# Optimization experiments

Measured on AMD Instinct MI355X. Metric: run time of the kernel, lower is better.

The kernel has to match this reference:

```python
import jax, jax.numpy as jnp
import numpy as np

N, DIM, T, V = 32, 256, 120, 25
H, HD = 8, 32            # num_heads, head_dim
MAX_HOP = 4
SCALE = HD ** -0.5


def setup_inputs() -> dict:
    key = jax.random.key(0)
    ks = jax.random.split(key, 9)
    x = jax.random.normal(ks[0], (N, DIM, T, V), jnp.float32)
    e = jax.random.normal(ks[1], (N, DIM, T, V), jnp.float32)
    # 1x1 conv weights (trunc_normal std=0.02 in the original init)
    W_kv = jax.random.normal(ks[2], (2 * DIM, DIM), jnp.float32) * 0.02
    W_q = jax.random.normal(ks[3], (DIM, DIM), jnp.float32) * 0.02
    W_proj = jax.random.normal(ks[4], (DIM, DIM), jnp.float32) * 0.02
    b_proj = jnp.zeros((DIM,), jnp.float32)
    rpe = jax.random.normal(ks[5], (MAX_HOP + 1, DIM), jnp.float32) * 0.02
    w1 = jax.random.normal(ks[6], (H, HD), jnp.float32) * 0.02
    # outer initialized as per-head identity (plus noise so grads are interesting)
    outer = jnp.broadcast_to(jnp.eye(V, dtype=jnp.float32), (H, V, V)) \
        + 0.1 * jax.random.normal(ks[7], (H, V, V), jnp.float32)
    alpha = 0.1 * jax.random.normal(ks[8], (1,), jnp.float32)
    idx = jnp.arange(V)
    hops = jnp.minimum(jnp.abs(idx[:, None] - idx[None, :]), MAX_HOP).astype(jnp.int32)
    return dict(x=x, e=e, W_kv=W_kv, W_q=W_q, W_proj=W_proj, b_proj=b_proj,
                rpe=rpe, w1=w1, outer=outer, alpha=alpha, hops=hops)


def reference(x, e, W_kv, W_q, W_proj, b_proj, rpe, w1, outer, alpha, hops):
    n, c, t, v = x.shape
    # 1x1 convs == channel matmuls
    kv = jnp.einsum('nctv,dc->ndtv', x, W_kv)                    # [N,2*DIM,T,V]
    kv = kv.reshape(n, 2, H, HD, t, v).transpose(1, 0, 4, 2, 5, 3)  # [2,N,T,H,V,HD]
    k, vv = kv[0], kv[1]
    q = jnp.einsum('nctv,dc->ndtv', x, W_q)
    q = q.reshape(n, H, HD, t, v).transpose(0, 3, 1, 4, 2)       # [N,T,H,V,HD]
    # content score
    attn = jnp.einsum('bthnc,bthmc->bthnm', q, k)                # [N,T,H,V,V]
    # hop relative-position bias
    k_r = rpe[hops].reshape(v, v, H, HD)                         # [V,V,H,HD]
    attn = attn + jnp.einsum('bthnc,nmhc->bthnm', q, k_r)
    # group term
    e_k = e.reshape(n, H, HD, t, v).transpose(0, 3, 1, 4, 2)     # [N,T,H,V,HD]
    attn = attn + jnp.einsum('bthnc,bthmc->bthnm', q, e_k)
    # group bias (broadcast over query index)
    attn = attn + jnp.einsum('hc,bthmc->bthm', w1, e_k)[..., None, :]
    attn = jax.nn.softmax(attn * SCALE, axis=-1)
    # outer/adjacency fusion then weighted V
    out = jnp.einsum('bthnm,bthmc->bthnc', alpha[0] * attn + outer, vv)
    # [N,T,H,V,HD] -> [N,T,H,HD,V] -> [N,T,DIM,V] -> [N,DIM,T,V]
    out = out.transpose(0, 1, 2, 4, 3).reshape(n, t, H * HD, v).transpose(0, 2, 1, 3)
    out = jnp.einsum('nctv,dc->ndtv', out, W_proj) + b_proj[None, :, None, None]
    return out
```

## Files before the change

### kernel.cpp

```cpp
#include <hip/hip_runtime.h>

typedef __attribute__((ext_vector_type(8))) short bf16x8;
typedef __attribute__((ext_vector_type(4))) float f32x4;
typedef unsigned short u16;
typedef unsigned int u32;

#define SCALE_ 0.17677669529663687f
#define MFMA(a,b,c) __builtin_amdgcn_mfma_f32_16x16x32_bf16(a,b,c,0,0,0)

__device__ __forceinline__ u16 f2bf(float f){
    u32 u = __float_as_uint(f);
    u = (u + 0x7FFFu + ((u >> 16) & 1u)) >> 16;
    return (u16)u;
}
__device__ __forceinline__ float bf2f(u32 h){ return __uint_as_float(h << 16); }
__device__ __forceinline__ u32 pk2(float a, float b){ return (u32)f2bf(a) | ((u32)f2bf(b) << 16); }

__device__ __forceinline__ bf16x8 frag8(uint2 p0, uint2 p1, int kg, int l15){
    const int s0 = ((kg & 1) << 5) + l15;
    const int s1 = s0 + 16;
    u32 a0 = (u32)__shfl((int)p0.x, s0, 64);
    u32 a1 = (u32)__shfl((int)p0.y, s0, 64);
    u32 a2 = (u32)__shfl((int)p0.x, s1, 64);
    u32 a3 = (u32)__shfl((int)p0.y, s1, 64);
    u32 b0 = (u32)__shfl((int)p1.x, s0, 64);
    u32 b1 = (u32)__shfl((int)p1.y, s0, 64);
    u32 b2 = (u32)__shfl((int)p1.x, s1, 64);
    u32 b3 = (u32)__shfl((int)p1.y, s1, 64);
    const bool hi = (kg >= 2);
    union { u32 u[4]; bf16x8 v; } r;
    r.u[0] = hi ? b0 : a0; r.u[1] = hi ? b1 : a1;
    r.u[2] = hi ? b2 : a2; r.u[3] = hi ? b3 : a3;
    return r.v;
}

#define PG_OFF_ 333312
#define NPAGES_ ((size_t)3840*8*2624)
#define BIAS_U16_ (PG_OFF_ + NPAGES_)

__global__ void prep_kernel(const float* __restrict__ Wkv, const float* __restrict__ Wq,
                            const float* __restrict__ Wproj, const float* __restrict__ rpe,
                            const float* __restrict__ w1, u16* __restrict__ wpk)
{
    int i = blockIdx.x * 256 + threadIdx.x;
    if (i < 65536)        wpk[i] = f2bf(Wq[i]);
    else if (i < 196608)  wpk[i] = f2bf(Wkv[i - 65536]);
    else if (i < 262144)  wpk[i] = f2bf(Wproj[i - 196608]);
    else if (i < 263424){
        int j = i - 262144;
        int jj = j >> 8, h = (j >> 5) & 7, hd = j & 31;
        wpk[i] = f2bf(rpe[jj*256 + h*32 + hd]);
    }
    else if (i < 263680)  wpk[i] = f2bf(w1[i - 263424]);
    else if (i < 267776){
        int j = i - 263680;
        int r = j >> 8, c = j & 255;
        float v = (r < 8 && (c >> 5) == r) ? w1[r*32 + (c & 31)] : 0.f;
        wpk[i] = f2bf(v);
    }
    else if (i < 333312){
        int j = i - 267776;
        int h = j >> 13;
        int r = j & 8191;
        int coct = r >> 8, hd = (r >> 3) & 31, clo = r & 7;
        wpk[i] = f2bf(Wkv[(size_t)(256 + h*32 + hd) * 256 + coct*8 + clo]);
    }
}

__launch_bounds__(512)
__global__ void qkv_gemm(const float* __restrict__ x, const float* __restrict__ e,
                         const u16* __restrict__ wpk, u16* __restrict__ pages,
                         float* __restrict__ bias_ws)
{
    __shared__ __align__(16) u16 xt[25664];

    const int tid = threadIdx.x;
    const int w = tid >> 6, lane = tid & 63;
    const int l15 = lane & 15, kg = lane >> 4;
    const int wg = ((int)blockIdx.x & 7) * 360 + ((int)blockIdx.x >> 3);
    const int sec = wg / 960, cb = wg % 960;
    const int n = cb / 30, tg = cb % 30;
    const f32x4 zf = {0.f, 0.f, 0.f, 0.f};

    const float* xb = x + (size_t)n*768000 + tg*100;
    for (int i = tid; i < 3200; i += 512){
        int col = i % 100, coct = i / 100;
        const float* xc = xb + (size_t)(coct*8)*3000 + col;
        u32 p[4];
        #pragma unroll
        for (int r = 0; r < 4; ++r)
            p[r] = pk2(xc[(2*r)*3000], xc[(2*r+1)*3000]);
        *(uint4*)&xt[(coct*100 + col)*8] = *(const uint4*)p;
    }
    __syncthreads();

    f32x4 acc[2][8];
    #pragma unroll
    for (int m = 0; m < 2; ++m)
        #pragma unroll
        for (int f = 0; f < 8; ++f) acc[m][f] = zf;

    const u16* wrow = wpk + (size_t)(sec*256 + w*32 + l15) * 256;
    #pragma unroll
    for (int ks = 0; ks < 8; ++ks){
        bf16x8 a0 = *(const bf16x8*)(wrow + ks*32 + kg*8);
        bf16x8 a1 = *(const bf16x8*)(wrow + 4096 + ks*32 + kg*8);
        #pragma unroll
        for (int f = 0; f < 8; ++f){
            int col = (f>>1)*25 + (f&1)*16 + l15;
            bf16x8 b = *(const bf16x8*)&xt[((ks*4+kg)*100 + col)*8];
            acc[0][f] = MFMA(a0, b, acc[0][f]);
            acc[1][f] = MFMA(a1, b, acc[1][f]);
        }
    }

    if (sec == 1){
        __syncthreads();
        const float* ebp = e + (size_t)n*768000 + tg*100;
        for (int i = tid; i < 3200; i += 512){
            int col = i % 100, coct = i / 100;
            const float* ec = ebp + (size_t)(coct*8)*3000 + col;
            u32 p[4];
            #pragma unroll
            for (int r = 0; r < 4; ++r)
                p[r] = pk2(ec[(2*r)*3000], ec[(2*r+1)*3000]);
            *(uint4*)&xt[(coct*100 + col)*8] = *(const uint4*)p;
        }
        __syncthreads();
        #pragma unroll
        for (int m = 0; m < 2; ++m){
            int c0 = w*32 + m*16 + kg*4;
            #pragma unroll
            for (int f = 0; f < 8; ++f){
                int col = (f>>1)*25 + (f&1)*16 + l15;
                uint2 ev = *(const uint2*)&xt[((c0>>3)*100 + col)*8 + (c0&7)];
                acc[m][f][0] += bf2f(ev.x & 0xFFFFu);
                acc[m][f][1] += bf2f(ev.x >> 16);
                acc[m][f][2] += bf2f(ev.y & 0xFFFFu);
                acc[m][f][3] += bf2f(ev.y >> 16);
            }
        }
    }

    const int secoff = (sec == 0) ? 0 : (sec == 1 ? 800 : 1600);
    #pragma unroll
    for (int m = 0; m < 2; ++m){
        #pragma unroll
        for (int f = 0; f < 8; ++f){
            int tt = f >> 1, a = (f&1)*16 + l15;
            if (a < 25){
                size_t nt = (size_t)(n*120 + tg*4 + tt);
                u16* pg = pages + (nt*8 + w)*2624 + secoff;
                int hd0 = m*16 + kg*4;
                if (sec < 2){
                    uint2 val; val.x = pk2(acc[m][f][0], acc[m][f][1]);
                    val.y = pk2(acc[m][f][2], acc[m][f][3]);
                    *(uint2*)&pg[((hd0>>3)*25 + a)*8 + (hd0&7)] = val;
                } else {
                    #pragma unroll
                    for (int r = 0; r < 4; ++r)
                        pg[((a>>3)*32 + hd0 + r)*8 + (a&7)] = f2bf(acc[m][f][r]);
                }
            }
        }
    }

    if (sec == 1 && w == 0){
        f32x4 bacc[8];
        #pragma unroll
        for (int f = 0; f < 8; ++f) bacc[f] = zf;
        const u16* w1f = wpk + 263680 + l15*256;
        #pragma unroll
        for (int ks = 0; ks < 8; ++ks){
            bf16x8 a = *(const bf16x8*)(w1f + ks*32 + kg*8);
            #pragma unroll
            for (int f = 0; f < 8; ++f){
                int col = (f>>1)*25 + (f&1)*16 + l15;
                bf16x8 b = *(const bf16x8*)&xt[((ks*4+kg)*100 + col)*8];
                bacc[f] = MFMA(a, b, bacc[f]);
            }
        }
        if (kg < 2){
            #pragma unroll
            for (int f = 0; f < 8; ++f){
                int tt = f >> 1, a = (f&1)*16 + l15;
                if (a < 25){
                    int nt = n*120 + tg*4 + tt;
                    #pragma unroll
                    for (int r = 0; r < 4; ++r)
                        bias_ws[(size_t)nt*256 + (kg*4+r)*32 + a] = bacc[f][r];
                }
            }
        }
    }
}

__launch_bounds__(512)
__global__ void attn_proj(const float* __restrict__ outer, const float* __restrict__ alpha,
                          const float* __restrict__ bproj, const u16* __restrict__ wpk,
                          const u16* __restrict__ pages, const float* __restrict__ bias_ws,
                          float* __restrict__ out)
{
    __shared__ __align__(16) u16 opk[6656 + 64];

    const int tid = threadIdx.x;
    const int w = tid >> 6, lane = tid & 63;
    const int l15 = lane & 15, kg = lane >> 4;
    const int wg = ((int)blockIdx.x & 7) * 480 + ((int)blockIdx.x >> 3);
    const int n = wg / 120, t = wg % 120;
    const float alpha0 = alpha[0];
    const f32x4 zf = {0.f, 0.f, 0.f, 0.f};
    const int h = w;
    const u16* pg = pages + ((size_t)wg*8 + h)*2624;

    bf16x8 fq0  = *(const bf16x8*)&pg[(kg*25 + l15)*8];
    bf16x8 fq1  = *(const bf16x8*)&pg[(kg*25 + 16 + l15)*8];
    bf16x8 fke0 = *(const bf16x8*)&pg[800 + (kg*25 + l15)*8];
    bf16x8 fke1;
    if (l15 < 9)       fke1 = *(const bf16x8*)&pg[800 + (kg*25 + 16 + l15)*8];
    else if (l15 <= 13) fke1 = *(const bf16x8*)(wpk + 262144 + ((l15-9)*8 + h)*32 + kg*8);
    else { union { u32 u[4]; bf16x8 v; } z; z.u[0]=z.u[1]=z.u[2]=z.u[3]=0; fke1 = z.v; }

    f32x4 sc[2][2];
    sc[0][0] = MFMA(fke0, fq0, zf);
    sc[0][1] = MFMA(fke0, fq1, zf);
    sc[1][0] = MFMA(fke1, fq0, zf);
    sc[1][1] = MFMA(fke1, fq1, zf);

    float bias01[2];
    bias01[0] = bias_ws[(size_t)wg*256 + h*32 + l15];
    bias01[1] = bias_ws[(size_t)wg*256 + h*32 + 16 + l15];

    uint2 P_G[2][2];
    #pragma unroll
    for (int nt = 0; nt < 2; ++nt){
        const int a = nt*16 + l15;
        f32x4 s0 = sc[0][nt], s1 = sc[1][nt];
        float rr0 = __shfl(s1[1], 32 + l15, 64);
        float rr1 = __shfl(s1[2], 32 + l15, 64);
        float rr2 = __shfl(s1[3], 32 + l15, 64);
        float rr3 = __shfl(s1[0], 48 + l15, 64);
        float rr4 = __shfl(s1[1], 48 + l15, 64);
        float tv[8];
        #pragma unroll
        for (int mt = 0; mt < 2; ++mt)
            #pragma unroll
            for (int r = 0; r < 4; ++r){
                int b = mt*16 + kg*4 + r;
                float sval = mt ? s1[r] : s0[r];
                float bb = __shfl(bias01[mt], (lane & 48) + (b & 15), 64);
                int d = a - b; d = d < 0 ? -d : d; if (d > 4) d = 4;
                float rj = d==0?rr0 : d==1?rr1 : d==2?rr2 : d==3?rr3 : rr4;
                float tt = (sval + rj + bb) * SCALE_;
                tv[mt*4+r] = (b < 25) ? tt : -1e30f;
            }
        float m = tv[0];
        #pragma unroll
        for (int i = 1; i < 8; ++i) m = fmaxf(m, tv[i]);
        m = fmaxf(m, __shfl_xor(m, 16, 64));
        m = fmaxf(m, __shfl_xor(m, 32, 64));
        float ex[8], sm = 0.f;
        #pragma unroll
        for (int i = 0; i < 8; ++i){ ex[i] = __expf(tv[i] - m); sm += ex[i]; }
        sm += __shfl_xor(sm, 16, 64);
        sm += __shfl_xor(sm, 32, 64);
        const float inv = alpha0 / sm;
        float g[8];
        #pragma unroll
        for (int mt = 0; mt < 2; ++mt)
            #pragma unroll
            for (int r = 0; r < 4; ++r){
                int b = mt*16 + kg*4 + r;
                float ov = (a < 25 && b < 25) ? outer[((size_t)h*25 + a)*25 + b] : 0.f;
                g[mt*4+r] = (b < 25) ? ex[mt*4+r]*inv + ov : 0.f;
            }
        uint2 pg0; pg0.x = pk2(g[0], g[1]); pg0.y = pk2(g[2], g[3]);
        uint2 pg1; pg1.x = pk2(g[4], g[5]); pg1.y = pk2(g[6], g[7]);
        P_G[nt][0] = pg0; P_G[nt][1] = pg1;
    }

    {
        bf16x8 fv0 = *(const bf16x8*)&pg[1600 + (kg*32 + l15)*8];
        bf16x8 fv1 = *(const bf16x8*)&pg[1600 + (kg*32 + 16 + l15)*8];
        bf16x8 fg0 = frag8(P_G[0][0], P_G[0][1], kg, l15);
        bf16x8 fg1 = frag8(P_G[1][0], P_G[1][1], kg, l15);
        f32x4 o[2][2];
        o[0][0] = MFMA(fv0, fg0, zf); o[0][1] = MFMA(fv0, fg1, zf);
        o[1][0] = MFMA(fv1, fg0, zf); o[1][1] = MFMA(fv1, fg1, zf);
        #pragma unroll
        for (int mt = 0; mt < 2; ++mt)
            #pragma unroll
            for (int nt = 0; nt < 2; ++nt){
                int a = nt*16 + l15;
                if (a < 25){
                    int coct = h*4 + mt*2 + (kg>>1);
                    u32* dst = (u32*)&opk[(coct*26 + a)*8 + (kg&1)*4];
                    dst[0] = pk2(o[mt][nt][0], o[mt][nt][1]);
                    dst[1] = pk2(o[mt][nt][2], o[mt][nt][3]);
                }
            }
    }
    __syncthreads();

    {
        f32x4 pc[2][2];
        #pragma unroll
        for (int i = 0; i < 2; ++i){ pc[i][0] = zf; pc[i][1] = zf; }
        #pragma unroll
        for (int ks = 0; ks < 8; ++ks){
            bf16x8 pb0 = *(const bf16x8*)&opk[((ks*4+kg)*26 + l15)*8];
            bf16x8 pb1 = *(const bf16x8*)&opk[((ks*4+kg)*26 + 16 + l15)*8];
            #pragma unroll
            for (int i = 0; i < 2; ++i){
                bf16x8 aw = *(const bf16x8*)(wpk + 196608 +
                                (size_t)(w*32 + i*16 + l15)*256 + ks*32 + kg*8);
                pc[i][0] = MFMA(aw, pb0, pc[i][0]);
                pc[i][1] = MFMA(aw, pb1, pc[i][1]);
            }
        }
        #pragma unroll
        for (int i = 0; i < 2; ++i){
            const int d = w*32 + i*16 + kg*4;
            float b0 = bproj[d], b1 = bproj[d+1], b2 = bproj[d+2], b3 = bproj[d+3];
            #pragma unroll
            for (int nt = 0; nt < 2; ++nt){
                int v = nt*16 + l15;
                if (v < 25){
                    float* op = out + (size_t)n*768000 + (size_t)d*3000 + t*25 + v;
                    op[0]    = pc[i][nt][0] + b0;
                    op[3000] = pc[i][nt][1] + b1;
                    op[6000] = pc[i][nt][2] + b2;
                    op[9000] = pc[i][nt][3] + b3;
                }
            }
        }
    }
}

__launch_bounds__(512, 4)
__global__ void mhsa_main(const float* __restrict__ x, const float* __restrict__ e,
                          const float* __restrict__ outer, const float* __restrict__ alpha,
                          const float* __restrict__ bproj, const u16* __restrict__ wpk,
                          float* __restrict__ out)
{
    __shared__ __align__(16) u16 smem[6656*3 + 64];
    u16* xs  = smem;
    u16* es  = smem + 6656;
    u16* opk = smem + 13312;

    const int tid = threadIdx.x;
    const int w = tid >> 6, lane = tid & 63;
    const int l15 = lane & 15, kg = lane >> 4;
    const int wg = (blockIdx.x & 7) * 480 + (blockIdx.x >> 3);
    const int n = wg / 120, t = wg % 120;
    const float alpha0 = alpha[0];
    const f32x4 zf = {0.f, 0.f, 0.f, 0.f};

    const float* xb = x + (size_t)n*768000 + t*25;
    const float* eb = e + (size_t)n*768000 + t*25;
    for (int i = tid; i < 6400; i += 512){
        int c = i / 25, v = i - c*25;
        int a16 = ((c>>3)*26 + v)*8 + (c&7);
        xs[a16] = f2bf(xb[c*3000 + v]);
        es[a16] = f2bf(eb[c*3000 + v]);
    }
    __syncthreads();

    {
        const int h = w;
        f32x4 cq[2][2], ck[2][2];
        #pragma unroll
        for (int i = 0; i < 2; ++i)
            #pragma unroll
            for (int j = 0; j < 2; ++j){ cq[i][j] = zf; ck[i][j] = zf; }
        {
            const u16* wq0 = wpk + (size_t)(h*32 + l15)*256;
            const u16* wk0 = wpk + 65536 + (size_t)(h*32 + l15)*256;
            #pragma unroll
            for (int ks = 0; ks < 8; ++ks){
                bf16x8 b0 = *(const bf16x8*)&xs[((ks*4+kg)*26 + l15)*8];
                bf16x8 b1 = *(const bf16x8*)&xs[((ks*4+kg)*26 + 16 + l15)*8];
                bf16x8 aq0 = *(const bf16x8*)(wq0 + ks*32 + kg*8);
                bf16x8 aq1 = *(const bf16x8*)(wq0 + 4096 + ks*32 + kg*8);
                bf16x8 ak0 = *(const bf16x8*)(wk0 + ks*32 + kg*8);
                bf16x8 ak1 = *(const bf16x8*)(wk0 + 4096 + ks*32 + kg*8);
                cq[0][0]=MFMA(aq0,b0,cq[0][0]); cq[0][1]=MFMA(aq0,b1,cq[0][1]);
                cq[1][0]=MFMA(aq1,b0,cq[1][0]); cq[1][1]=MFMA(aq1,b1,cq[1][1]);
                ck[0][0]=MFMA(ak0,b0,ck[0][0]); ck[0][1]=MFMA(ak0,b1,ck[0][1]);
                ck[1][0]=MFMA(ak1,b0,ck[1][0]); ck[1][1]=MFMA(ak1,b1,ck[1][1]);
            }
        }
        uint2 P_q[2][2], P_k[2][2];
        #pragma unroll
        for (int mt = 0; mt < 2; ++mt)
            #pragma unroll
            for (int nt = 0; nt < 2; ++nt){
                int coct = h*4 + mt*2 + (kg>>1);
                uint2 ev = *(const uint2*)&es[(coct*26 + nt*16 + l15)*8 + (kg&1)*4];
                ck[mt][nt][0] += bf2f(ev.x & 0xFFFFu);
                ck[mt][nt][1] += bf2f(ev.x >> 16);
                ck[mt][nt][2] += bf2f(ev.y & 0xFFFFu);
                ck[mt][nt][3] += bf2f(ev.y >> 16);
                uint2 pq; pq.x = pk2(cq[mt][nt][0], cq[mt][nt][1]);
                pq.y = pk2(cq[mt][nt][2], cq[mt][nt][3]);
                P_q[nt][mt] = pq;
                uint2 pk; pk.x = pk2(ck[mt][nt][0], ck[mt][nt][1]);
                pk.y = pk2(ck[mt][nt][2], ck[mt][nt][3]);
                P_k[nt][mt] = pk;
            }
        float bias01[2];
        {
            bf16x8 aw1 = *(const bf16x8*)(wpk + 263424 + h*32 + kg*8);
            bf16x8 be0 = *(const bf16x8*)&es[((h*4+kg)*26 + l15)*8];
            bf16x8 be1 = *(const bf16x8*)&es[((h*4+kg)*26 + 16 + l15)*8];
            f32x4 cb0 = MFMA(aw1, be0, zf);
            f32x4 cb1 = MFMA(aw1, be1, zf);
            bias01[0] = cb0[0]; bias01[1] = cb1[0];
        }
        f32x4 cv[2][2];
        #pragma unroll
        for (int i = 0; i < 2; ++i)
            #pragma unroll
            for (int j = 0; j < 2; ++j) cv[i][j] = zf;
        {
            const u16* wvt = wpk + 267776 + h*8192;
            #pragma unroll
            for (int ks = 0; ks < 8; ++ks){
                bf16x8 a0 = *(const bf16x8*)&xs[((ks*4+kg)*26 + l15)*8];
                bf16x8 a1 = *(const bf16x8*)&xs[((ks*4+kg)*26 + 16 + l15)*8];
                bf16x8 bv0 = *(const bf16x8*)&wvt[((ks*4+kg)*32 + l15)*8];
                bf16x8 bv1 = *(const bf16x8*)&wvt[((ks*4+kg)*32 + 16 + l15)*8];
                cv[0][0]=MFMA(a0,bv0,cv[0][0]); cv[0][1]=MFMA(a0,bv1,cv[0][1]);
                cv[1][0]=MFMA(a1,bv0,cv[1][0]); cv[1][1]=MFMA(a1,bv1,cv[1][1]);
            }
        }
        #pragma unroll
        for (int nt = 0; nt < 2; ++nt)
            #pragma unroll
            for (int r = 0; r < 4; ++r)
                cv[1][nt][r] = (kg*4 + r < 9) ? cv[1][nt][r] : 0.f;
        uint2 P_v[2][2];
        #pragma unroll
        for (int mt = 0; mt < 2; ++mt)
            #pragma unroll
            for (int nt = 0; nt < 2; ++nt){
                uint2 pv; pv.x = pk2(cv[mt][nt][0], cv[mt][nt][1]);
                pv.y = pk2(cv[mt][nt][2], cv[mt][nt][3]);
                P_v[nt][mt] = pv;
            }
        bf16x8 fq0  = frag8(P_q[0][0], P_q[0][1], kg, l15);
        bf16x8 fq1  = frag8(P_q[1][0], P_q[1][1], kg, l15);
        bf16x8 fke0 = frag8(P_k[0][0], P_k[0][1], kg, l15);
        bf16x8 fke1 = frag8(P_k[1][0], P_k[1][1], kg, l15);
        if (l15 >= 9){
            if (l15 <= 13)
                fke1 = *(const bf16x8*)(wpk + 262144 + ((l15-9)*8 + h)*32 + kg*8);
            else {
                union { u32 u[4]; bf16x8 v; } z; z.u[0]=z.u[1]=z.u[2]=z.u[3]=0;
                fke1 = z.v;
            }
        }
        f32x4 sc[2][2];
        sc[0][0] = MFMA(fke0, fq0, zf);
        sc[0][1] = MFMA(fke0, fq1, zf);
        sc[1][0] = MFMA(fke1, fq0, zf);
        sc[1][1] = MFMA(fke1, fq1, zf);
        uint2 P_G[2][2];
        #pragma unroll
        for (int nt = 0; nt < 2; ++nt){
            const int a = nt*16 + l15;
            f32x4 s0 = sc[0][nt], s1 = sc[1][nt];
            float rr0 = __shfl(s1[1], 32 + l15, 64);
            float rr1 = __shfl(s1[2], 32 + l15, 64);
            float rr2 = __shfl(s1[3], 32 + l15, 64);
            float rr3 = __shfl(s1[0], 48 + l15, 64);
            float rr4 = __shfl(s1[1], 48 + l15, 64);
            float tv[8];
            #pragma unroll
            for (int mt = 0; mt < 2; ++mt)
                #pragma unroll
                for (int r = 0; r < 4; ++r){
                    int b = mt*16 + kg*4 + r;
                    float sval = mt ? s1[r] : s0[r];
                    float bb = __shfl(bias01[mt], (lane & 48) + (b & 15), 64);
                    int d = a - b; d = d < 0 ? -d : d; if (d > 4) d = 4;
                    float rj = d==0?rr0 : d==1?rr1 : d==2?rr2 : d==3?rr3 : rr4;
                    float tt = (sval + rj + bb) * SCALE_;
                    tv[mt*4+r] = (b < 25) ? tt : -1e30f;
                }
            float m = tv[0];
            #pragma unroll
            for (int i = 1; i < 8; ++i) m = fmaxf(m, tv[i]);
            m = fmaxf(m, __shfl_xor(m, 16, 64));
            m = fmaxf(m, __shfl_xor(m, 32, 64));
            float ex[8], sm = 0.f;
            #pragma unroll
            for (int i = 0; i < 8; ++i){ ex[i] = __expf(tv[i] - m); sm += ex[i]; }
            sm += __shfl_xor(sm, 16, 64);
            sm += __shfl_xor(sm, 32, 64);
            const float inv = alpha0 / sm;
            float g[8];
            #pragma unroll
            for (int mt = 0; mt < 2; ++mt)
                #pragma unroll
                for (int r = 0; r < 4; ++r){
                    int b = mt*16 + kg*4 + r;
                    float ov = (a < 25 && b < 25) ? outer[((size_t)h*25 + a)*25 + b] : 0.f;
                    g[mt*4+r] = (b < 25) ? ex[mt*4+r]*inv + ov : 0.f;
                }
            uint2 pg0; pg0.x = pk2(g[0], g[1]); pg0.y = pk2(g[2], g[3]);
            uint2 pg1; pg1.x = pk2(g[4], g[5]); pg1.y = pk2(g[6], g[7]);
            P_G[nt][0] = pg0; P_G[nt][1] = pg1;
        }
        {
            bf16x8 fv0 = frag8(P_v[0][0], P_v[0][1], kg, l15);
            bf16x8 fv1 = frag8(P_v[1][0], P_v[1][1], kg, l15);
            bf16x8 fg0 = frag8(P_G[0][0], P_G[0][1], kg, l15);
            bf16x8 fg1 = frag8(P_G[1][0], P_G[1][1], kg, l15);
            f32x4 o[2][2];
            o[0][0] = MFMA(fv0, fg0, zf); o[0][1] = MFMA(fv0, fg1, zf);
            o[1][0] = MFMA(fv1, fg0, zf); o[1][1] = MFMA(fv1, fg1, zf);
            #pragma unroll
            for (int mt = 0; mt < 2; ++mt)
                #pragma unroll
                for (int nt = 0; nt < 2; ++nt){
                    int a = nt*16 + l15;
                    if (a < 25){
                        int coct = h*4 + mt*2 + (kg>>1);
                        u32* dst = (u32*)&opk[(coct*26 + a)*8 + (kg&1)*4];
                        dst[0] = pk2(o[mt][nt][0], o[mt][nt][1]);
                        dst[1] = pk2(o[mt][nt][2], o[mt][nt][3]);
                    }
                }
        }
    }
    __syncthreads();

    {
        f32x4 pc[2][2];
        #pragma unroll
        for (int i = 0; i < 2; ++i){ pc[i][0] = zf; pc[i][1] = zf; }
        #pragma unroll
        for (int ks = 0; ks < 8; ++ks){
            bf16x8 pb0 = *(const bf16x8*)&opk[((ks*4+kg)*26 + l15)*8];
            bf16x8 pb1 = *(const bf16x8*)&opk[((ks*4+kg)*26 + 16 + l15)*8];
            #pragma unroll
            for (int i = 0; i < 2; ++i){
                bf16x8 aw = *(const bf16x8*)(wpk + 196608 +
                                (size_t)(w*32 + i*16 + l15)*256 + ks*32 + kg*8);
                pc[i][0] = MFMA(aw, pb0, pc[i][0]);
                pc[i][1] = MFMA(aw, pb1, pc[i][1]);
            }
        }
        #pragma unroll
        for (int i = 0; i < 2; ++i){
            const int d = w*32 + i*16 + kg*4;
            float b0 = bproj[d], b1 = bproj[d+1], b2 = bproj[d+2], b3 = bproj[d+3];
            #pragma unroll
            for (int nt = 0; nt < 2; ++nt){
                int v = nt*16 + l15;
                if (v < 25){
                    float* op = out + (size_t)n*768000 + (size_t)d*3000 + t*25 + v;
                    op[0]    = pc[i][nt][0] + b0;
                    op[3000] = pc[i][nt][1] + b1;
                    op[6000] = pc[i][nt][2] + b2;
                    op[9000] = pc[i][nt][3] + b3;
                }
            }
        }
    }
}

extern "C" void kernel_launch(void* const* d_in, const int* in_sizes, int n_in,
                              void* d_out, int out_size, void* d_ws, size_t ws_size,
                              hipStream_t stream) {
    (void)in_sizes; (void)n_in; (void)out_size;
    const float* x     = (const float*)d_in[0];
    const float* e     = (const float*)d_in[1];
    const float* Wkv   = (const float*)d_in[2];
    const float* Wq    = (const float*)d_in[3];
    const float* Wproj = (const float*)d_in[4];
    const float* bproj = (const float*)d_in[5];
    const float* rpe   = (const float*)d_in[6];
    const float* w1    = (const float*)d_in[7];
    const float* outer = (const float*)d_in[8];
    const float* alpha = (const float*)d_in[9];
    float* out = (float*)d_out;
    u16* wpk = (u16*)d_ws;

    prep_kernel<<<1302, 256, 0, stream>>>(Wkv, Wq, Wproj, rpe, w1, wpk);

    const size_t need = (size_t)BIAS_U16_ * 2 + (size_t)3840*256*4 + 4096;
    if (ws_size >= need){
        u16* pages = wpk + PG_OFF_;
        float* bias_ws = (float*)(wpk + BIAS_U16_);
        qkv_gemm<<<2880, 512, 0, stream>>>(x, e, wpk, pages, bias_ws);
        attn_proj<<<3840, 512, 0, stream>>>(outer, alpha, bproj, wpk, pages, bias_ws, out);
    } else {
        mhsa_main<<<3840, 512, 0, stream>>>(x, e, outer, alpha, bproj, wpk, out);
    }
}
```

Baseline: 278.8 us.

## Split qkv_gemm into smaller 30-column, half-head-range blocks for more parallelism

Restructures the QKV projection kernel so each 256-thread block handles 30 flattened (t,v) columns and half of the output channels of one section, instead of 100 columns and all channels with 512 threads. The grid grows from 2880 to 19200 blocks and LDS per block shrinks, aiming for higher occupancy and better load balance. It also adds occupancy hints to launch_bounds on both kernels. In exchange, each x/e tile is now loaded and converted six times across sections and halves, raising global read traffic, and MFMA work per block is much smaller.

```diff
diff --git a/kernel.cpp b/kernel.cpp
--- a/kernel.cpp
+++ b/kernel.cpp
@@ -67,48 +67,48 @@
     }
 }
 
-__launch_bounds__(512)
+__launch_bounds__(256, 8)
 __global__ void qkv_gemm(const float* __restrict__ x, const float* __restrict__ e,
                          const u16* __restrict__ wpk, u16* __restrict__ pages,
                          float* __restrict__ bias_ws)
 {
-    __shared__ __align__(16) u16 xt[25664];
+    __shared__ __align__(16) u16 xt[7696];
 
     const int tid = threadIdx.x;
     const int w = tid >> 6, lane = tid & 63;
     const int l15 = lane & 15, kg = lane >> 4;
-    const int wg = ((int)blockIdx.x & 7) * 360 + ((int)blockIdx.x >> 3);
-    const int sec = wg / 960, cb = wg % 960;
-    const int n = cb / 30, tg = cb % 30;
+    const int wg = ((int)blockIdx.x & 7) * 2400 + ((int)blockIdx.x >> 3);
+    const int n = wg / 600, rr = wg % 600;
+    const int tg = rr / 6, sr = rr % 6;
+    const int sec = sr >> 1, h2 = sr & 1;
     const f32x4 zf = {0.f, 0.f, 0.f, 0.f};
 
-    const float* xb = x + (size_t)n*768000 + tg*100;
-    for (int i = tid; i < 3200; i += 512){
-        int col = i % 100, coct = i / 100;
+    const float* xb = x + (size_t)n*768000 + tg*30;
+    for (int i = tid; i < 960; i += 256){
+        int col = i % 30, coct = i / 30;
         const float* xc = xb + (size_t)(coct*8)*3000 + col;
         u32 p[4];
         #pragma unroll
-        for (int r = 0; r < 4; ++r)
-            p[r] = pk2(xc[(2*r)*3000], xc[(2*r+1)*3000]);
-        *(uint4*)&xt[(coct*100 + col)*8] = *(const uint4*)p;
+        for (int r2 = 0; r2 < 4; ++r2)
+            p[r2] = pk2(xc[(2*r2)*3000], xc[(2*r2+1)*3000]);
+        *(uint4*)&xt[(coct*30 + col)*8] = *(const uint4*)p;
     }
     __syncthreads();
 
-    f32x4 acc[2][8];
+    f32x4 acc[2][2];
     #pragma unroll
     for (int m = 0; m < 2; ++m)
         #pragma unroll
-        for (int f = 0; f < 8; ++f) acc[m][f] = zf;
-
-    const u16* wrow = wpk + (size_t)(sec*256 + w*32 + l15) * 256;
+        for (int f = 0; f < 2; ++f) acc[m][f] = zf;
+
+    const u16* wrow = wpk + (size_t)(sec*256 + h2*128 + w*32 + l15) * 256;
     #pragma unroll
     for (int ks = 0; ks < 8; ++ks){
         bf16x8 a0 = *(const bf16x8*)(wrow + ks*32 + kg*8);
         bf16x8 a1 = *(const bf16x8*)(wrow + 4096 + ks*32 + kg*8);
         #pragma unroll
-        for (int f = 0; f < 8; ++f){
-            int col = (f>>1)*25 + (f&1)*16 + l15;
-            bf16x8 b = *(const bf16x8*)&xt[((ks*4+kg)*100 + col)*8];
+        for (int f = 0; f < 2; ++f){
+            bf16x8 b = *(const bf16x8*)&xt[((ks*4+kg)*30 + f*16 + l15)*8];
             acc[0][f] = MFMA(a0, b, acc[0][f]);
             acc[1][f] = MFMA(a1, b, acc[1][f]);
         }
@@ -116,24 +116,23 @@
 
     if (sec == 1){
         __syncthreads();
-        const float* ebp = e + (size_t)n*768000 + tg*100;
-        for (int i = tid; i < 3200; i += 512){
-            int col = i % 100, coct = i / 100;
+        const float* ebp = e + (size_t)n*768000 + tg*30;
+        for (int i = tid; i < 960; i += 256){
+            int col = i % 30, coct = i / 30;
             const float* ec = ebp + (size_t)(coct*8)*3000 + col;
             u32 p[4];
             #pragma unroll
-            for (int r = 0; r < 4; ++r)
-                p[r] = pk2(ec[(2*r)*3000], ec[(2*r+1)*3000]);
-            *(uint4*)&xt[(coct*100 + col)*8] = *(const uint4*)p;
+            for (int r2 = 0; r2 < 4; ++r2)
+                p[r2] = pk2(ec[(2*r2)*3000], ec[(2*r2+1)*3000]);
+            *(uint4*)&xt[(coct*30 + col)*8] = *(const uint4*)p;
         }
         __syncthreads();
         #pragma unroll
         for (int m = 0; m < 2; ++m){
-            int c0 = w*32 + m*16 + kg*4;
-            #pragma unroll
-            for (int f = 0; f < 8; ++f){
-                int col = (f>>1)*25 + (f&1)*16 + l15;
-                uint2 ev = *(const uint2*)&xt[((c0>>3)*100 + col)*8 + (c0&7)];
+            int c0 = h2*128 + w*32 + m*16 + kg*4;
+            #pragma unroll
+            for (int f = 0; f < 2; ++f){
+                uint2 ev = *(const uint2*)&xt[((c0>>3)*30 + f*16 + l15)*8 + (c0&7)];
                 acc[m][f][0] += bf2f(ev.x & 0xFFFFu);
                 acc[m][f][1] += bf2f(ev.x >> 16);
                 acc[m][f][2] += bf2f(ev.y & 0xFFFFu);
@@ -143,14 +142,17 @@
     }
 
     const int secoff = (sec == 0) ? 0 : (sec == 1 ? 800 : 1600);
+    const int h = h2*4 + w;
     #pragma unroll
     for (int m = 0; m < 2; ++m){
         #pragma unroll
-        for (int f = 0; f < 8; ++f){
-            int tt = f >> 1, a = (f&1)*16 + l15;
-            if (a < 25){
-                size_t nt = (size_t)(n*120 + tg*4 + tt);
-                u16* pg = pages + (nt*8 + w)*2624 + secoff;
+        for (int f = 0; f < 2; ++f){
+            int sl = f*16 + l15;
+            if (sl < 30){
+                int c  = tg*30 + sl;
+                int tt = c / 25, a = c - tt*25;
+                size_t nt = (size_t)(n*120 + tt);
+                u16* pg = pages + (nt*8 + h)*2624 + secoff;
                 int hd0 = m*16 + kg*4;
                 if (sec < 2){
                     uint2 val; val.x = pk2(acc[m][f][0], acc[m][f][1]);
@@ -158,44 +160,43 @@
                     *(uint2*)&pg[((hd0>>3)*25 + a)*8 + (hd0&7)] = val;
                 } else {
                     #pragma unroll
-                    for (int r = 0; r < 4; ++r)
-                        pg[((a>>3)*32 + hd0 + r)*8 + (a&7)] = f2bf(acc[m][f][r]);
-                }
-            }
-        }
-    }
-
-    if (sec == 1 && w == 0){
-        f32x4 bacc[8];
-        #pragma unroll
-        for (int f = 0; f < 8; ++f) bacc[f] = zf;
+                    for (int r2 = 0; r2 < 4; ++r2)
+                        pg[((a>>3)*32 + hd0 + r2)*8 + (a&7)] = f2bf(acc[m][f][r2]);
+                }
+            }
+        }
+    }
+
+    if (sec == 1 && h2 == 0 && w == 0){
+        f32x4 bacc[2];
+        bacc[0] = zf; bacc[1] = zf;
         const u16* w1f = wpk + 263680 + l15*256;
         #pragma unroll
         for (int ks = 0; ks < 8; ++ks){
             bf16x8 a = *(const bf16x8*)(w1f + ks*32 + kg*8);
             #pragma unroll
-            for (int f = 0; f < 8; ++f){
-                int col = (f>>1)*25 + (f&1)*16 + l15;
-                bf16x8 b = *(const bf16x8*)&xt[((ks*4+kg)*100 + col)*8];
+            for (int f = 0; f < 2; ++f){
+                bf16x8 b = *(const bf16x8*)&xt[((ks*4+kg)*30 + f*16 + l15)*8];
                 bacc[f] = MFMA(a, b, bacc[f]);
             }
         }
         if (kg < 2){
             #pragma unroll
-            for (int f = 0; f < 8; ++f){
-                int tt = f >> 1, a = (f&1)*16 + l15;
-                if (a < 25){
-                    int nt = n*120 + tg*4 + tt;
+            for (int f = 0; f < 2; ++f){
+                int sl = f*16 + l15;
+                if (sl < 30){
+                    int c = tg*30 + sl;
+                    int tt = c / 25, a = c - tt*25;
                     #pragma unroll
-                    for (int r = 0; r < 4; ++r)
-                        bias_ws[(size_t)nt*256 + (kg*4+r)*32 + a] = bacc[f][r];
+                    for (int r2 = 0; r2 < 4; ++r2)
+                        bias_ws[(size_t)(n*120 + tt)*256 + (kg*4+r2)*32 + a] = bacc[f][r2];
                 }
             }
         }
     }
 }
 
-__launch_bounds__(512)
+__launch_bounds__(512, 4)
 __global__ void attn_proj(const float* __restrict__ outer, const float* __restrict__ alpha,
                           const float* __restrict__ bproj, const u16* __restrict__ wpk,
                           const u16* __restrict__ pages, const float* __restrict__ bias_ws,
@@ -594,7 +595,7 @@
     if (ws_size >= need){
         u16* pages = wpk + PG_OFF_;
         float* bias_ws = (float*)(wpk + BIAS_U16_);
-        qkv_gemm<<<2880, 512, 0, stream>>>(x, e, wpk, pages, bias_ws);
+        qkv_gemm<<<19200, 256, 0, stream>>>(x, e, wpk, pages, bias_ws);
         attn_proj<<<3840, 512, 0, stream>>>(outer, alpha, bproj, wpk, pages, bias_ws, out);
     } else {
         mhsa_main<<<3840, 512, 0, stream>>>(x, e, outer, alpha, bproj, wpk, out);
```

Measured after the change: 376.0 us. +34.9%, slower.

## Compute q, k, v sections in one block to reuse staged x and e tiles

Applied to the files above, without the earlier changes.

The QKV projection kernel now stages both x and e for a 2-timestep tile into shared memory once and loops over all three output sections inside the block. Previously each block computed only one section for 4 timesteps, so x was read from global memory and converted to bf16 three times. This cuts global input traffic and conversion work, at the cost of fewer blocks, smaller MFMA tiles per section and more serial work per block.

```diff
diff --git a/kernel.cpp b/kernel.cpp
--- a/kernel.cpp
+++ b/kernel.cpp
@@ -72,120 +72,113 @@
                          const u16* __restrict__ wpk, u16* __restrict__ pages,
                          float* __restrict__ bias_ws)
 {
-    __shared__ __align__(16) u16 xt[25664];
+    __shared__ __align__(16) u16 xs[12864];
+    __shared__ __align__(16) u16 es[12864];
 
     const int tid = threadIdx.x;
     const int w = tid >> 6, lane = tid & 63;
     const int l15 = lane & 15, kg = lane >> 4;
-    const int wg = ((int)blockIdx.x & 7) * 360 + ((int)blockIdx.x >> 3);
-    const int sec = wg / 960, cb = wg % 960;
-    const int n = cb / 30, tg = cb % 30;
+    const int wg = ((int)blockIdx.x & 7) * 240 + ((int)blockIdx.x >> 3);
+    const int n = wg / 60, tg = wg % 60;
     const f32x4 zf = {0.f, 0.f, 0.f, 0.f};
 
-    const float* xb = x + (size_t)n*768000 + tg*100;
+    const float* xb = x + (size_t)n*768000 + tg*50;
+    const float* eb = e + (size_t)n*768000 + tg*50;
     for (int i = tid; i < 3200; i += 512){
-        int col = i % 100, coct = i / 100;
-        const float* xc = xb + (size_t)(coct*8)*3000 + col;
+        int j = i < 1600 ? i : i - 1600;
+        int col = j % 50, coct = j / 50;
+        const float* src = (i < 1600 ? xb : eb) + (size_t)(coct*8)*3000 + col;
         u32 p[4];
         #pragma unroll
         for (int r = 0; r < 4; ++r)
-            p[r] = pk2(xc[(2*r)*3000], xc[(2*r+1)*3000]);
-        *(uint4*)&xt[(coct*100 + col)*8] = *(const uint4*)p;
+            p[r] = pk2(src[(2*r)*3000], src[(2*r+1)*3000]);
+        u16* dst = (i < 1600 ? xs : es);
+        *(uint4*)&dst[(coct*50 + col)*8] = *(const uint4*)p;
     }
     __syncthreads();
 
-    f32x4 acc[2][8];
-    #pragma unroll
-    for (int m = 0; m < 2; ++m)
-        #pragma unroll
-        for (int f = 0; f < 8; ++f) acc[m][f] = zf;
-
-    const u16* wrow = wpk + (size_t)(sec*256 + w*32 + l15) * 256;
-    #pragma unroll
-    for (int ks = 0; ks < 8; ++ks){
-        bf16x8 a0 = *(const bf16x8*)(wrow + ks*32 + kg*8);
-        bf16x8 a1 = *(const bf16x8*)(wrow + 4096 + ks*32 + kg*8);
-        #pragma unroll
-        for (int f = 0; f < 8; ++f){
-            int col = (f>>1)*25 + (f&1)*16 + l15;
-            bf16x8 b = *(const bf16x8*)&xt[((ks*4+kg)*100 + col)*8];
-            acc[0][f] = MFMA(a0, b, acc[0][f]);
-            acc[1][f] = MFMA(a1, b, acc[1][f]);
-        }
-    }
-
-    if (sec == 1){
-        __syncthreads();
-        const float* ebp = e + (size_t)n*768000 + tg*100;
-        for (int i = tid; i < 3200; i += 512){
-            int col = i % 100, coct = i / 100;
-            const float* ec = ebp + (size_t)(coct*8)*3000 + col;
-            u32 p[4];
-            #pragma unroll
-            for (int r = 0; r < 4; ++r)
-                p[r] = pk2(ec[(2*r)*3000], ec[(2*r+1)*3000]);
-            *(uint4*)&xt[(coct*100 + col)*8] = *(const uint4*)p;
-        }
-        __syncthreads();
+    for (int sec = 0; sec < 3; ++sec){
+        f32x4 acc[2][4];
+        #pragma unroll
+        for (int m = 0; m < 2; ++m)
+            #pragma unroll
+            for (int f = 0; f < 4; ++f) acc[m][f] = zf;
+
+        const u16* wrow = wpk + (size_t)(sec*256 + w*32 + l15) * 256;
+        #pragma unroll
+        for (int ks = 0; ks < 8; ++ks){
+            bf16x8 a0 = *(const bf16x8*)(wrow + ks*32 + kg*8);
+            bf16x8 a1 = *(const bf16x8*)(wrow + 4096 + ks*32 + kg*8);
+            #pragma unroll
+            for (int f = 0; f < 4; ++f){
+                int col = (f>>1)*25 + (f&1)*16 + l15;
+                bf16x8 b = *(const bf16x8*)&xs[((ks*4+kg)*50 + col)*8];
+                acc[0][f] = MFMA(a0, b, acc[0][f]);
+                acc[1][f] = MFMA(a1, b, acc[1][f]);
+            }
+        }
+
+        if (sec == 1){
+            #pragma unroll
+            for (int m = 0; m < 2; ++m){
+                int c0 = w*32 + m*16 + kg*4;
+                #pragma unroll
+                for (int f = 0; f < 4; ++f){
+                    int col = (f>>1)*25 + (f&1)*16 + l15;
+                    uint2 ev = *(const uint2*)&es[((c0>>3)*50 + col)*8 + (c0&7)];
+                    acc[m][f][0] += bf2f(ev.x & 0xFFFFu);
+                    acc[m][f][1] += bf2f(ev.x >> 16);
+                    acc[m][f][2] += bf2f(ev.y & 0xFFFFu);
+                    acc[m][f][3] += bf2f(ev.y >> 16);
+                }
+            }
+        }
+
+        const int secoff = (sec == 0) ? 0 : (sec == 1 ? 800 : 1600);
         #pragma unroll
         for (int m = 0; m < 2; ++m){
-            int c0 = w*32 + m*16 + kg*4;
-            #pragma unroll
-            for (int f = 0; f < 8; ++f){
-                int col = (f>>1)*25 + (f&1)*16 + l15;
-                uint2 ev = *(const uint2*)&xt[((c0>>3)*100 + col)*8 + (c0&7)];
-                acc[m][f][0] += bf2f(ev.x & 0xFFFFu);
-                acc[m][f][1] += bf2f(ev.x >> 16);
-                acc[m][f][2] += bf2f(ev.y & 0xFFFFu);
-                acc[m][f][3] += bf2f(ev.y >> 16);
-            }
-        }
-    }
-
-    const int secoff = (sec == 0) ? 0 : (sec == 1 ? 800 : 1600);
-    #pragma unroll
-    for (int m = 0; m < 2; ++m){
-        #pragma unroll
-        for (int f = 0; f < 8; ++f){
-            int tt = f >> 1, a = (f&1)*16 + l15;
-            if (a < 25){
-                size_t nt = (size_t)(n*120 + tg*4 + tt);
-                u16* pg = pages + (nt*8 + w)*2624 + secoff;
-                int hd0 = m*16 + kg*4;
-                if (sec < 2){
-                    uint2 val; val.x = pk2(acc[m][f][0], acc[m][f][1]);
-                    val.y = pk2(acc[m][f][2], acc[m][f][3]);
-                    *(uint2*)&pg[((hd0>>3)*25 + a)*8 + (hd0&7)] = val;
-                } else {
-                    #pragma unroll
-                    for (int r = 0; r < 4; ++r)
-                        pg[((a>>3)*32 + hd0 + r)*8 + (a&7)] = f2bf(acc[m][f][r]);
-                }
-            }
-        }
-    }
-
-    if (sec == 1 && w == 0){
-        f32x4 bacc[8];
-        #pragma unroll
-        for (int f = 0; f < 8; ++f) bacc[f] = zf;
+            int hd0 = m*16 + kg*4;
+            #pragma unroll
+            for (int f = 0; f < 4; ++f){
+                int tt = f >> 1, a = (f&1)*16 + l15;
+                if (a < 25){
+                    size_t nt = (size_t)(n*120 + tg*2 + tt);
+                    u16* pg = pages + (nt*8 + w)*2624 + secoff;
+                    if (sec < 2){
+                        uint2 val; val.x = pk2(acc[m][f][0], acc[m][f][1]);
+                        val.y = pk2(acc[m][f][2], acc[m][f][3]);
+                        *(uint2*)&pg[((hd0>>3)*25 + a)*8 + (hd0&7)] = val;
+                    } else {
+                        #pragma unroll
+                        for (int r = 0; r < 4; ++r)
+                            pg[((a>>3)*32 + hd0 + r)*8 + (a&7)] = f2bf(acc[m][f][r]);
+                    }
+                }
+            }
+        }
+    }
+
+    if (w == 0){
+        f32x4 bacc[4];
+        #pragma unroll
+        for (int f = 0; f < 4; ++f) bacc[f] = zf;
         const u16* w1f = wpk + 263680 + l15*256;
         #pragma unroll
         for (int ks = 0; ks < 8; ++ks){
             bf16x8 a = *(const bf16x8*)(w1f + ks*32 + kg*8);
             #pragma unroll
-            for (int f = 0; f < 8; ++f){
+            for (int f = 0; f < 4; ++f){
                 int col = (f>>1)*25 + (f&1)*16 + l15;
-                bf16x8 b = *(const bf16x8*)&xt[((ks*4+kg)*100 + col)*8];
+                bf16x8 b = *(const bf16x8*)&es[((ks*4+kg)*50 + col)*8];
                 bacc[f] = MFMA(a, b, bacc[f]);
             }
         }
         if (kg < 2){
             #pragma unroll
-            for (int f = 0; f < 8; ++f){
+            for (int f = 0; f < 4; ++f){
                 int tt = f >> 1, a = (f&1)*16 + l15;
                 if (a < 25){
-                    int nt = n*120 + tg*4 + tt;
+                    int nt = n*120 + tg*2 + tt;
                     #pragma unroll
                     for (int r = 0; r < 4; ++r)
                         bias_ws[(size_t)nt*256 + (kg*4+r)*32 + a] = bacc[f][r];
@@ -594,7 +587,7 @@
     if (ws_size >= need){
         u16* pages = wpk + PG_OFF_;
         float* bias_ws = (float*)(wpk + BIAS_U16_);
-        qkv_gemm<<<2880, 512, 0, stream>>>(x, e, wpk, pages, bias_ws);
+        qkv_gemm<<<1920, 512, 0, stream>>>(x, e, wpk, pages, bias_ws);
         attn_proj<<<3840, 512, 0, stream>>>(outer, alpha, bproj, wpk, pages, bias_ws, out);
     } else {
         mhsa_main<<<3840, 512, 0, stream>>>(x, e, outer, alpha, bproj, wpk, out);
```

After: 287.6 us. 3.2% more time.
